# Performance work log

Hardware: AMD Instinct MI355X
Metric: run time of the kernel (lower is better)

## Reference

```python
import jax, jax.numpy as jnp
import numpy as np


def setup_inputs() -> dict:
    key = jax.random.key(0)
    ks = jax.random.split(key, 8)
    B, C, H, W = 32, 98, 128, 128
    F, D = 256, 128
    return {
        "hm": jax.random.normal(ks[0], (B, C, H, W), dtype=jnp.float32),
        "feat": jax.random.normal(ks[1], (B, F, H, W), dtype=jnp.float32),
        "W_embed": jax.random.normal(ks[2], (2 + 1 + F, D), dtype=jnp.float32) * 0.05,
        "b_embed": jax.random.normal(ks[3], (D,), dtype=jnp.float32) * 0.05,
        "A": jax.random.normal(ks[4], (C, C), dtype=jnp.float32) * 0.05,
        "W_gcn": jax.random.normal(ks[5], (D, D), dtype=jnp.float32) * 0.05,
        "W_out": jax.random.normal(ks[6], (D, 2), dtype=jnp.float32) * 0.05,
        "b_out": jax.random.normal(ks[7], (2,), dtype=jnp.float32) * 0.05,
    }


def reference(hm, feat, W_embed, b_embed, A, W_gcn, W_out, b_out):
    # hm: [B, C, H, W] per-landmark heatmaps; feat: [B, F, H, W] backbone features.
    B, C, H, W = hm.shape
    F = feat.shape[1]

    # decode_heatmap: per-(batch, landmark) argmax location over HxW (batched,
    # replacing the original per-sample Python loops).
    hm_flat = hm.reshape(B, C, H * W)
    idx = jnp.argmax(hm_flat, axis=-1)                      # [B, C] int
    ys = idx // W
    xs = idx % W

    # node confidences: hm[i, classIds, ys, xs] -> batched gather
    conf = jnp.take_along_axis(hm_flat, idx[:, :, None], axis=-1)[..., 0]  # [B, C]

    # pooling_feature: gather the F-dim feature vector at each landmark location
    feat_flat = feat.reshape(B, F, H * W)
    vis = jnp.take_along_axis(feat_flat, idx[:, None, :], axis=-1)  # [B, F, C]
    vis = jnp.transpose(vis, (0, 2, 1))                              # [B, C, F]

    # normalized positions: node_positions (x, y) / hm_size [h, w] (as in source)
    hm_size = jnp.array([H, W], dtype=hm.dtype)
    pos = jnp.stack([xs, ys], axis=-1).astype(hm.dtype) / hm_size    # [B, C, 2]

    # GCN over landmarks (batched instead of per-sample calls)
    node = jnp.concatenate([pos, conf[..., None], vis], axis=-1)     # [B, C, 2+1+F]
    h0 = jax.nn.relu(jnp.einsum("bcf,fd->bcd", node, W_embed) + b_embed)
    h1 = jax.nn.relu(jnp.einsum("ij,bjd,de->bie", A, h0, W_gcn))     # learned adjacency
    out = jnp.einsum("bcd,do->bco", h1, W_out) + b_out               # [B, C, 2]
    return hm, out
```

## Files before the change

### kernel.cpp

```cpp
#include <hip/hip_runtime.h>

#define HM_B 32
#define HM_C 98
#define HM_H 128
#define HM_W 128
#define HWSZ (HM_H * HM_W)
#define FDIM 256
#define DDIM 128
#define NODE_F (2 + 1 + FDIM)
#define BC (HM_B * HM_C)
#define HM_ELEMS ((size_t)BC * HWSZ)
#define LCHUNK 8
#define ICHUNK 7

typedef float f32x4 __attribute__((ext_vector_type(4)));

__global__ __launch_bounds__(256) void argmax_copy_kernel(
    const float* __restrict__ hm, float* __restrict__ out_hm,
    int* __restrict__ idx_ws, float* __restrict__ conf_ws) {
    const int bc = blockIdx.x;
    const int tid = threadIdx.x;
    const f32x4* __restrict__ src = (const f32x4*)(hm + (size_t)bc * HWSZ);
    f32x4* __restrict__ dst = (f32x4*)(out_hm + (size_t)bc * HWSZ);

    float bv = -INFINITY;
    int bi = 0;
    #pragma unroll
    for (int t = 0; t < HWSZ / 4 / 256; ++t) {
        const int p = t * 256 + tid;
        const f32x4 v = __builtin_nontemporal_load(src + p);
        __builtin_nontemporal_store(v, dst + p);
        const float m4 = fmaxf(fmaxf(v[0], v[1]), fmaxf(v[2], v[3]));
        if (m4 > bv) {
            const int base = p * 4;
            if (v[0] > bv) { bv = v[0]; bi = base; }
            if (v[1] > bv) { bv = v[1]; bi = base + 1; }
            if (v[2] > bv) { bv = v[2]; bi = base + 2; }
            if (v[3] > bv) { bv = v[3]; bi = base + 3; }
        }
    }

    __shared__ float sv[256];
    __shared__ int si[256];
    sv[tid] = bv; si[tid] = bi;
    __syncthreads();
    for (int s = 128; s > 0; s >>= 1) {
        if (tid < s) {
            const float ov = sv[tid + s];
            const int oi = si[tid + s];
            if (ov > sv[tid] || (ov == sv[tid] && oi < si[tid])) {
                sv[tid] = ov; si[tid] = oi;
            }
        }
        __syncthreads();
    }
    if (tid == 0) { idx_ws[bc] = si[0]; conf_ws[bc] = sv[0]; }
}

__global__ __launch_bounds__(256) void embed_kernel(
    const float* __restrict__ feat, const int* __restrict__ idx_ws,
    const float* __restrict__ conf_ws, const float* __restrict__ W_embed,
    const float* __restrict__ b_embed, float* __restrict__ h0) {
    const int bc0 = blockIdx.x * LCHUNK;
    const int tid = threadIdx.x;
    __shared__ float node_s[LCHUNK][NODE_F + 1];

    if (tid < LCHUNK) {
        const int bcL = bc0 + tid;
        const int loc = idx_ws[bcL];
        const int ys = loc / HM_W;
        const int xs = loc % HM_W;
        node_s[tid][0] = (float)xs / (float)HM_H;
        node_s[tid][1] = (float)ys / (float)HM_W;
        node_s[tid][2] = conf_ws[bcL];
    }
    #pragma unroll
    for (int l = 0; l < LCHUNK; ++l) {
        const int bcL = bc0 + l;
        const int b = bcL / HM_C;
        const int loc = idx_ws[bcL];
        node_s[l][3 + tid] = feat[((size_t)(b * FDIM + tid)) * HWSZ + loc];
    }
    __syncthreads();

    const int d = tid & (DDIM - 1);
    const int lbase = (tid >> 7) * 4;
    const float bias = b_embed[d];
    float acc0 = bias, acc1 = bias, acc2 = bias, acc3 = bias;
    for (int f = 0; f < NODE_F; ++f) {
        const float w = W_embed[f * DDIM + d];
        acc0 = fmaf(node_s[lbase + 0][f], w, acc0);
        acc1 = fmaf(node_s[lbase + 1][f], w, acc1);
        acc2 = fmaf(node_s[lbase + 2][f], w, acc2);
        acc3 = fmaf(node_s[lbase + 3][f], w, acc3);
    }
    h0[(size_t)(bc0 + lbase + 0) * DDIM + d] = fmaxf(acc0, 0.f);
    h0[(size_t)(bc0 + lbase + 1) * DDIM + d] = fmaxf(acc1, 0.f);
    h0[(size_t)(bc0 + lbase + 2) * DDIM + d] = fmaxf(acc2, 0.f);
    h0[(size_t)(bc0 + lbase + 3) * DDIM + d] = fmaxf(acc3, 0.f);
}

__global__ __launch_bounds__(128) void gcn_kernel(
    const float* __restrict__ A, const float* __restrict__ h0,
    const float* __restrict__ W_gcn, const float* __restrict__ W_out,
    const float* __restrict__ b_out, float* __restrict__ out2) {
    const int b = blockIdx.x / (HM_C / ICHUNK);
    const int i0 = (blockIdx.x % (HM_C / ICHUNK)) * ICHUNK;
    const int tid = threadIdx.x;

    __shared__ float h0_s[HM_C * DDIM];
    __shared__ float tmp_s[ICHUNK * DDIM];
    __shared__ float h1_s[ICHUNK * DDIM];

    for (int j = 0; j < HM_C; ++j)
        h0_s[j * DDIM + tid] = h0[((size_t)b * HM_C + j) * DDIM + tid];
    __syncthreads();

    {
        float acc[ICHUNK];
        #pragma unroll
        for (int i = 0; i < ICHUNK; ++i) acc[i] = 0.f;
        for (int j = 0; j < HM_C; ++j) {
            const float v = h0_s[j * DDIM + tid];
            #pragma unroll
            for (int i = 0; i < ICHUNK; ++i)
                acc[i] = fmaf(A[(i0 + i) * HM_C + j], v, acc[i]);
        }
        #pragma unroll
        for (int i = 0; i < ICHUNK; ++i) tmp_s[i * DDIM + tid] = acc[i];
    }
    __syncthreads();

    {
        float acc[ICHUNK];
        #pragma unroll
        for (int i = 0; i < ICHUNK; ++i) acc[i] = 0.f;
        for (int k = 0; k < DDIM; ++k) {
            const float w = W_gcn[k * DDIM + tid];
            #pragma unroll
            for (int i = 0; i < ICHUNK; ++i)
                acc[i] = fmaf(tmp_s[i * DDIM + k], w, acc[i]);
        }
        #pragma unroll
        for (int i = 0; i < ICHUNK; ++i) h1_s[i * DDIM + tid] = fmaxf(acc[i], 0.f);
    }
    __syncthreads();

    if (tid < ICHUNK * 2) {
        const int i = tid >> 1;
        const int o = tid & 1;
        float acc = b_out[o];
        for (int dd = 0; dd < DDIM; ++dd)
            acc = fmaf(h1_s[i * DDIM + dd], W_out[dd * 2 + o], acc);
        out2[((size_t)b * HM_C + i0 + i) * 2 + o] = acc;
    }
}

extern "C" void kernel_launch(void* const* d_in, const int* in_sizes, int n_in,
                              void* d_out, int out_size, void* d_ws, size_t ws_size,
                              hipStream_t stream) {
    const float* hm      = (const float*)d_in[0];
    const float* feat    = (const float*)d_in[1];
    const float* W_embed = (const float*)d_in[2];
    const float* b_embed = (const float*)d_in[3];
    const float* A       = (const float*)d_in[4];
    const float* W_gcn   = (const float*)d_in[5];
    const float* W_out   = (const float*)d_in[6];
    const float* b_out   = (const float*)d_in[7];

    float* out_hm = (float*)d_out;
    float* out2   = (float*)d_out + HM_ELEMS;

    char* ws = (char*)d_ws;
    int*   idx_ws  = (int*)ws;    ws += BC * sizeof(int);
    float* conf_ws = (float*)ws;  ws += BC * sizeof(float);
    float* h0      = (float*)ws;

    argmax_copy_kernel<<<BC, 256, 0, stream>>>(hm, out_hm, idx_ws, conf_ws);
    embed_kernel<<<BC / LCHUNK, 256, 0, stream>>>(feat, idx_ws, conf_ws,
                                                  W_embed, b_embed, h0);
    gcn_kernel<<<HM_B * (HM_C / ICHUNK), 128, 0, stream>>>(A, h0, W_gcn,
                                                           W_out, b_out, out2);
}
```

Measured before the change: 128.5 us.

## Fuse argmax, embed and GCN stages into one cooperative persistent kernel

Replaces three kernel launches with a single cooperative kernel of 512 persistent blocks that loops over heatmap rows, then uses grid-wide syncs between the argmax/copy, embedding and GCN phases. The aim is to remove launch gaps and tail effects between stages. The GCN stage no longer stages all of h0 in shared memory; it caches only the needed A rows and reads h0 from global memory, which cuts shared memory use. Nontemporal loads and stores in the copy are also replaced with plain ones. Risks include the cost of grid syncs, fewer blocks in flight for the large copy, and cache pollution from the normal stores. The original three launches remain as a fallback if the cooperative launch fails.

New measurement: 268.0 us. 2.09x slower.

```diff
diff --git a/kernel.cpp b/kernel.cpp
--- a/kernel.cpp
+++ b/kernel.cpp
@@ -1,4 +1,7 @@
 #include <hip/hip_runtime.h>
+#include <hip/hip_cooperative_groups.h>
+
+namespace cg = cooperative_groups;
 
 #define HM_B 32
 #define HM_C 98
@@ -12,24 +15,24 @@
 #define HM_ELEMS ((size_t)BC * HWSZ)
 #define LCHUNK 8
 #define ICHUNK 7
+#define NBLK 512
+#define NTHR 256
 
 typedef float f32x4 __attribute__((ext_vector_type(4)));
 
-__global__ __launch_bounds__(256) void argmax_copy_kernel(
-    const float* __restrict__ hm, float* __restrict__ out_hm,
-    int* __restrict__ idx_ws, float* __restrict__ conf_ws) {
-    const int bc = blockIdx.x;
-    const int tid = threadIdx.x;
-    const f32x4* __restrict__ src = (const f32x4*)(hm + (size_t)bc * HWSZ);
-    f32x4* __restrict__ dst = (f32x4*)(out_hm + (size_t)bc * HWSZ);
-
+
+__device__ __forceinline__ void argmax_copy_row(
+    const float* __restrict__ hm, float* __restrict__ out_hm, int row, int tid,
+    float* sv, int* si, int* __restrict__ idx_ws, float* __restrict__ conf_ws) {
+    const f32x4* __restrict__ src = (const f32x4*)(hm + (size_t)row * HWSZ);
+    f32x4* __restrict__ dst = (f32x4*)(out_hm + (size_t)row * HWSZ);
     float bv = -INFINITY;
     int bi = 0;
     #pragma unroll
-    for (int t = 0; t < HWSZ / 4 / 256; ++t) {
-        const int p = t * 256 + tid;
-        const f32x4 v = __builtin_nontemporal_load(src + p);
-        __builtin_nontemporal_store(v, dst + p);
+    for (int t = 0; t < HWSZ / 4 / NTHR; ++t) {
+        const int p = t * NTHR + tid;
+        const f32x4 v = src[p];
+        dst[p] = v;
         const float m4 = fmaxf(fmaxf(v[0], v[1]), fmaxf(v[2], v[3]));
         if (m4 > bv) {
             const int base = p * 4;
@@ -39,12 +42,9 @@
             if (v[3] > bv) { bv = v[3]; bi = base + 3; }
         }
     }
-
-    __shared__ float sv[256];
-    __shared__ int si[256];
     sv[tid] = bv; si[tid] = bi;
     __syncthreads();
-    for (int s = 128; s > 0; s >>= 1) {
+    for (int s = NTHR / 2; s > 0; s >>= 1) {
         if (tid < s) {
             const float ov = sv[tid + s];
             const int oi = si[tid + s];
@@ -54,32 +54,31 @@
         }
         __syncthreads();
     }
-    if (tid == 0) { idx_ws[bc] = si[0]; conf_ws[bc] = sv[0]; }
-}
-
-__global__ __launch_bounds__(256) void embed_kernel(
+    if (tid == 0) { idx_ws[row] = si[0]; conf_ws[row] = sv[0]; }
+    __syncthreads();
+}
+
+__device__ __forceinline__ void embed_unit(
     const float* __restrict__ feat, const int* __restrict__ idx_ws,
     const float* __restrict__ conf_ws, const float* __restrict__ W_embed,
-    const float* __restrict__ b_embed, float* __restrict__ h0) {
-    const int bc0 = blockIdx.x * LCHUNK;
-    const int tid = threadIdx.x;
-    __shared__ float node_s[LCHUNK][NODE_F + 1];
-
+    const float* __restrict__ b_embed, float* __restrict__ h0,
+    int unit, int tid, float (*node)[NODE_F + 1]) {
+    const int bc0 = unit * LCHUNK;
+    #pragma unroll
+    for (int l = 0; l < LCHUNK; ++l) {
+        const int bcL = bc0 + l;
+        const int b = bcL / HM_C;
+        const int loc = idx_ws[bcL];
+        node[l][3 + tid] = feat[((size_t)(b * FDIM + tid)) * HWSZ + loc];
+    }
     if (tid < LCHUNK) {
         const int bcL = bc0 + tid;
         const int loc = idx_ws[bcL];
         const int ys = loc / HM_W;
         const int xs = loc % HM_W;
-        node_s[tid][0] = (float)xs / (float)HM_H;
-        node_s[tid][1] = (float)ys / (float)HM_W;
-        node_s[tid][2] = conf_ws[bcL];
-    }
-    #pragma unroll
-    for (int l = 0; l < LCHUNK; ++l) {
-        const int bcL = bc0 + l;
-        const int b = bcL / HM_C;
-        const int loc = idx_ws[bcL];
-        node_s[l][3 + tid] = feat[((size_t)(b * FDIM + tid)) * HWSZ + loc];
+        node[tid][0] = (float)xs / (float)HM_H;
+        node[tid][1] = (float)ys / (float)HM_W;
+        node[tid][2] = conf_ws[bcL];
     }
     __syncthreads();
 
@@ -89,49 +88,49 @@
     float acc0 = bias, acc1 = bias, acc2 = bias, acc3 = bias;
     for (int f = 0; f < NODE_F; ++f) {
         const float w = W_embed[f * DDIM + d];
-        acc0 = fmaf(node_s[lbase + 0][f], w, acc0);
-        acc1 = fmaf(node_s[lbase + 1][f], w, acc1);
-        acc2 = fmaf(node_s[lbase + 2][f], w, acc2);
-        acc3 = fmaf(node_s[lbase + 3][f], w, acc3);
+        acc0 = fmaf(node[lbase + 0][f], w, acc0);
+        acc1 = fmaf(node[lbase + 1][f], w, acc1);
+        acc2 = fmaf(node[lbase + 2][f], w, acc2);
+        acc3 = fmaf(node[lbase + 3][f], w, acc3);
     }
     h0[(size_t)(bc0 + lbase + 0) * DDIM + d] = fmaxf(acc0, 0.f);
     h0[(size_t)(bc0 + lbase + 1) * DDIM + d] = fmaxf(acc1, 0.f);
     h0[(size_t)(bc0 + lbase + 2) * DDIM + d] = fmaxf(acc2, 0.f);
     h0[(size_t)(bc0 + lbase + 3) * DDIM + d] = fmaxf(acc3, 0.f);
-}
-
-__global__ __launch_bounds__(128) void gcn_kernel(
+    __syncthreads();
+}
+
+__device__ __forceinline__ void gcn_unit(
     const float* __restrict__ A, const float* __restrict__ h0,
     const float* __restrict__ W_gcn, const float* __restrict__ W_out,
-    const float* __restrict__ b_out, float* __restrict__ out2) {
-    const int b = blockIdx.x / (HM_C / ICHUNK);
-    const int i0 = (blockIdx.x % (HM_C / ICHUNK)) * ICHUNK;
-    const int tid = threadIdx.x;
-
-    __shared__ float h0_s[HM_C * DDIM];
-    __shared__ float tmp_s[ICHUNK * DDIM];
-    __shared__ float h1_s[ICHUNK * DDIM];
-
-    for (int j = 0; j < HM_C; ++j)
-        h0_s[j * DDIM + tid] = h0[((size_t)b * HM_C + j) * DDIM + tid];
-    __syncthreads();
-
-    {
+    const float* __restrict__ b_out, float* __restrict__ out2,
+    int unit, int tid, char* smraw) {
+    float* arow  = (float*)smraw;
+    float* tmp_s = (float*)(smraw + 2752);
+    float* h1_s  = (float*)(smraw + 2752 + 3584);
+    const int b = unit / (HM_C / ICHUNK);
+    const int i0 = (unit % (HM_C / ICHUNK)) * ICHUNK;
+
+    for (int k = tid; k < ICHUNK * HM_C; k += NTHR)
+        arow[k] = A[(i0 + k / HM_C) * HM_C + (k % HM_C)];
+    __syncthreads();
+
+    if (tid < DDIM) {
         float acc[ICHUNK];
         #pragma unroll
         for (int i = 0; i < ICHUNK; ++i) acc[i] = 0.f;
         for (int j = 0; j < HM_C; ++j) {
-            const float v = h0_s[j * DDIM + tid];
+            const float v = h0[((size_t)b * HM_C + j) * DDIM + tid];
             #pragma unroll
             for (int i = 0; i < ICHUNK; ++i)
-                acc[i] = fmaf(A[(i0 + i) * HM_C + j], v, acc[i]);
+                acc[i] = fmaf(arow[i * HM_C + j], v, acc[i]);
         }
         #pragma unroll
         for (int i = 0; i < ICHUNK; ++i) tmp_s[i * DDIM + tid] = acc[i];
     }
     __syncthreads();
 
-    {
+    if (tid < DDIM) {
         float acc[ICHUNK];
         #pragma unroll
         for (int i = 0; i < ICHUNK; ++i) acc[i] = 0.f;
@@ -154,6 +153,63 @@
             acc = fmaf(h1_s[i * DDIM + dd], W_out[dd * 2 + o], acc);
         out2[((size_t)b * HM_C + i0 + i) * 2 + o] = acc;
     }
+    __syncthreads();
+}
+
+
+__global__ __launch_bounds__(NTHR, 2) void fused_kernel(
+    const float* __restrict__ hm, const float* __restrict__ feat,
+    const float* __restrict__ W_embed, const float* __restrict__ b_embed,
+    const float* __restrict__ A, const float* __restrict__ W_gcn,
+    const float* __restrict__ W_out, const float* __restrict__ b_out,
+    float* __restrict__ out_hm, float* __restrict__ out2,
+    int* __restrict__ idx_ws, float* __restrict__ conf_ws,
+    float* __restrict__ h0_ws) {
+    cg::grid_group grid = cg::this_grid();
+    const int tid = threadIdx.x;
+    __shared__ __align__(16) char smraw[10240];
+
+    {
+        float* sv = (float*)smraw;
+        int* si = (int*)(smraw + NTHR * sizeof(float));
+        for (int row = blockIdx.x; row < BC; row += NBLK)
+            argmax_copy_row(hm, out_hm, row, tid, sv, si, idx_ws, conf_ws);
+    }
+    grid.sync();
+
+    if (blockIdx.x < BC / LCHUNK)
+        embed_unit(feat, idx_ws, conf_ws, W_embed, b_embed, h0_ws,
+                   blockIdx.x, tid, (float (*)[NODE_F + 1])smraw);
+    grid.sync();
+
+    if (blockIdx.x < HM_B * (HM_C / ICHUNK))
+        gcn_unit(A, h0_ws, W_gcn, W_out, b_out, out2, blockIdx.x, tid, smraw);
+}
+
+
+__global__ __launch_bounds__(NTHR) void argmax_copy_kernel(
+    const float* __restrict__ hm, float* __restrict__ out_hm,
+    int* __restrict__ idx_ws, float* __restrict__ conf_ws) {
+    __shared__ float sv[NTHR];
+    __shared__ int si[NTHR];
+    argmax_copy_row(hm, out_hm, blockIdx.x, threadIdx.x, sv, si, idx_ws, conf_ws);
+}
+
+__global__ __launch_bounds__(NTHR) void embed_kernel(
+    const float* __restrict__ feat, const int* __restrict__ idx_ws,
+    const float* __restrict__ conf_ws, const float* __restrict__ W_embed,
+    const float* __restrict__ b_embed, float* __restrict__ h0) {
+    __shared__ float node[LCHUNK][NODE_F + 1];
+    embed_unit(feat, idx_ws, conf_ws, W_embed, b_embed, h0,
+               blockIdx.x, threadIdx.x, node);
+}
+
+__global__ __launch_bounds__(NTHR) void gcn_kernel(
+    const float* __restrict__ A, const float* __restrict__ h0,
+    const float* __restrict__ W_gcn, const float* __restrict__ W_out,
+    const float* __restrict__ b_out, float* __restrict__ out2) {
+    __shared__ __align__(16) char smraw[10240];
+    gcn_unit(A, h0, W_gcn, W_out, b_out, out2, blockIdx.x, threadIdx.x, smraw);
 }
 
 extern "C" void kernel_launch(void* const* d_in, const int* in_sizes, int n_in,
@@ -174,11 +230,21 @@
     char* ws = (char*)d_ws;
     int*   idx_ws  = (int*)ws;    ws += BC * sizeof(int);
     float* conf_ws = (float*)ws;  ws += BC * sizeof(float);
-    float* h0      = (float*)ws;
-
-    argmax_copy_kernel<<<BC, 256, 0, stream>>>(hm, out_hm, idx_ws, conf_ws);
-    embed_kernel<<<BC / LCHUNK, 256, 0, stream>>>(feat, idx_ws, conf_ws,
-                                                  W_embed, b_embed, h0);
-    gcn_kernel<<<HM_B * (HM_C / ICHUNK), 128, 0, stream>>>(A, h0, W_gcn,
-                                                           W_out, b_out, out2);
-}
+    float* h0_ws   = (float*)ws;
+
+    void* args[] = {(void*)&hm, (void*)&feat, (void*)&W_embed, (void*)&b_embed,
+                    (void*)&A, (void*)&W_gcn, (void*)&W_out, (void*)&b_out,
+                    (void*)&out_hm, (void*)&out2, (void*)&idx_ws, (void*)&conf_ws,
+                    (void*)&h0_ws};
+    hipError_t err = hipLaunchCooperativeKernel(
+        reinterpret_cast<void*>(fused_kernel), dim3(NBLK), dim3(NTHR),
+        args, 0, stream);
+
+    if (err != hipSuccess) {
+        argmax_copy_kernel<<<BC, NTHR, 0, stream>>>(hm, out_hm, idx_ws, conf_ws);
+        embed_kernel<<<BC / LCHUNK, NTHR, 0, stream>>>(feat, idx_ws, conf_ws,
+                                                       W_embed, b_embed, h0_ws);
+        gcn_kernel<<<HM_B * (HM_C / ICHUNK), NTHR, 0, stream>>>(
+            A, h0_ws, W_gcn, W_out, b_out, out2);
+    }
+}
```

## Fuse feature gather into argmax kernel and stage A rows in GCN shared memory

Applied to the files above, without the earlier changes.

The argmax/copy kernel now gathers the 256-dim feature vector at the argmax location itself and writes a full padded node row (position, confidence, features) to a workspace. The embed kernel then only loads these rows, and writes h0 back into the first 128 slots of the same rows. The GCN kernel drops the 50 KB shared-memory copy of h0, which should raise occupancy. It caches the block's rows of A in shared memory and reads h0 directly from global memory instead. In exchange, each argmax block ends with a tail of scattered feature loads, and the GCN's h0 reads go to global or cache instead of LDS.

After: 127.7 us. Within noise of the previous version (-0.6%).

```diff
diff --git a/kernel.cpp b/kernel.cpp
--- a/kernel.cpp
+++ b/kernel.cpp
@@ -8,26 +8,28 @@
 #define FDIM 256
 #define DDIM 128
 #define NODE_F (2 + 1 + FDIM)
+#define NODE_P 260
 #define BC (HM_B * HM_C)
 #define HM_ELEMS ((size_t)BC * HWSZ)
 #define LCHUNK 8
 #define ICHUNK 7
+#define NTHR 256
 
 typedef float f32x4 __attribute__((ext_vector_type(4)));
 
-__global__ __launch_bounds__(256) void argmax_copy_kernel(
-    const float* __restrict__ hm, float* __restrict__ out_hm,
-    int* __restrict__ idx_ws, float* __restrict__ conf_ws) {
-    const int bc = blockIdx.x;
+__global__ __launch_bounds__(NTHR) void k1_copy_argmax_gather(
+    const float* __restrict__ hm, const float* __restrict__ feat,
+    float* __restrict__ out_hm, float* __restrict__ node_ws) {
+    const int row = blockIdx.x;
     const int tid = threadIdx.x;
-    const f32x4* __restrict__ src = (const f32x4*)(hm + (size_t)bc * HWSZ);
-    f32x4* __restrict__ dst = (f32x4*)(out_hm + (size_t)bc * HWSZ);
+    const f32x4* __restrict__ src = (const f32x4*)(hm + (size_t)row * HWSZ);
+    f32x4* __restrict__ dst = (f32x4*)(out_hm + (size_t)row * HWSZ);
 
     float bv = -INFINITY;
     int bi = 0;
     #pragma unroll
-    for (int t = 0; t < HWSZ / 4 / 256; ++t) {
-        const int p = t * 256 + tid;
+    for (int t = 0; t < HWSZ / 4 / NTHR; ++t) {
+        const int p = t * NTHR + tid;
         const f32x4 v = __builtin_nontemporal_load(src + p);
         __builtin_nontemporal_store(v, dst + p);
         const float m4 = fmaxf(fmaxf(v[0], v[1]), fmaxf(v[2], v[3]));
@@ -40,11 +42,11 @@
         }
     }
 
-    __shared__ float sv[256];
-    __shared__ int si[256];
+    __shared__ float sv[NTHR];
+    __shared__ int si[NTHR];
     sv[tid] = bv; si[tid] = bi;
     __syncthreads();
-    for (int s = 128; s > 0; s >>= 1) {
+    for (int s = NTHR / 2; s > 0; s >>= 1) {
         if (tid < s) {
             const float ov = sv[tid + s];
             const int oi = si[tid + s];
@@ -54,66 +56,64 @@
         }
         __syncthreads();
     }
-    if (tid == 0) { idx_ws[bc] = si[0]; conf_ws[bc] = sv[0]; }
+
+    const int loc = si[0];
+    const float conf = sv[0];
+    const int b = row / HM_C;
+    const float vis = feat[((size_t)(b * FDIM + tid)) * HWSZ + loc];
+    float* nrow = node_ws + (size_t)row * NODE_P;
+    nrow[3 + tid] = vis;
+    if (tid == 0) {
+        nrow[0] = (float)(loc % HM_W) * (1.0f / (float)HM_H);
+        nrow[1] = (float)(loc / HM_W) * (1.0f / (float)HM_W);
+        nrow[2] = conf;
+    }
 }
 
-__global__ __launch_bounds__(256) void embed_kernel(
-    const float* __restrict__ feat, const int* __restrict__ idx_ws,
-    const float* __restrict__ conf_ws, const float* __restrict__ W_embed,
-    const float* __restrict__ b_embed, float* __restrict__ h0) {
+__global__ __launch_bounds__(NTHR) void k2_embed(
+    float* __restrict__ node_ws, const float* __restrict__ W_embed,
+    const float* __restrict__ b_embed) {
     const int bc0 = blockIdx.x * LCHUNK;
     const int tid = threadIdx.x;
-    __shared__ float node_s[LCHUNK][NODE_F + 1];
+    __shared__ float node_s[LCHUNK][NODE_P];
 
-    if (tid < LCHUNK) {
-        const int bcL = bc0 + tid;
-        const int loc = idx_ws[bcL];
-        const int ys = loc / HM_W;
-        const int xs = loc % HM_W;
-        node_s[tid][0] = (float)xs / (float)HM_H;
-        node_s[tid][1] = (float)ys / (float)HM_W;
-        node_s[tid][2] = conf_ws[bcL];
-    }
     #pragma unroll
-    for (int l = 0; l < LCHUNK; ++l) {
-        const int bcL = bc0 + l;
-        const int b = bcL / HM_C;
-        const int loc = idx_ws[bcL];
-        node_s[l][3 + tid] = feat[((size_t)(b * FDIM + tid)) * HWSZ + loc];
-    }
+    for (int l = 0; l < LCHUNK; ++l)
+        for (int k = tid; k < NODE_F; k += NTHR)
+            node_s[l][k] = node_ws[(size_t)(bc0 + l) * NODE_P + k];
     __syncthreads();
 
     const int d = tid & (DDIM - 1);
     const int lbase = (tid >> 7) * 4;
     const float bias = b_embed[d];
-    float acc0 = bias, acc1 = bias, acc2 = bias, acc3 = bias;
+    float a0 = bias, a1 = bias, a2 = bias, a3 = bias;
     for (int f = 0; f < NODE_F; ++f) {
         const float w = W_embed[f * DDIM + d];
-        acc0 = fmaf(node_s[lbase + 0][f], w, acc0);
-        acc1 = fmaf(node_s[lbase + 1][f], w, acc1);
-        acc2 = fmaf(node_s[lbase + 2][f], w, acc2);
-        acc3 = fmaf(node_s[lbase + 3][f], w, acc3);
+        a0 = fmaf(node_s[lbase + 0][f], w, a0);
+        a1 = fmaf(node_s[lbase + 1][f], w, a1);
+        a2 = fmaf(node_s[lbase + 2][f], w, a2);
+        a3 = fmaf(node_s[lbase + 3][f], w, a3);
     }
-    h0[(size_t)(bc0 + lbase + 0) * DDIM + d] = fmaxf(acc0, 0.f);
-    h0[(size_t)(bc0 + lbase + 1) * DDIM + d] = fmaxf(acc1, 0.f);
-    h0[(size_t)(bc0 + lbase + 2) * DDIM + d] = fmaxf(acc2, 0.f);
-    h0[(size_t)(bc0 + lbase + 3) * DDIM + d] = fmaxf(acc3, 0.f);
+    node_ws[(size_t)(bc0 + lbase + 0) * NODE_P + d] = fmaxf(a0, 0.f);
+    node_ws[(size_t)(bc0 + lbase + 1) * NODE_P + d] = fmaxf(a1, 0.f);
+    node_ws[(size_t)(bc0 + lbase + 2) * NODE_P + d] = fmaxf(a2, 0.f);
+    node_ws[(size_t)(bc0 + lbase + 3) * NODE_P + d] = fmaxf(a3, 0.f);
 }
 
-__global__ __launch_bounds__(128) void gcn_kernel(
-    const float* __restrict__ A, const float* __restrict__ h0,
+__global__ __launch_bounds__(DDIM) void k3_gcn(
+    const float* __restrict__ A, const float* __restrict__ node_ws,
     const float* __restrict__ W_gcn, const float* __restrict__ W_out,
     const float* __restrict__ b_out, float* __restrict__ out2) {
     const int b = blockIdx.x / (HM_C / ICHUNK);
     const int i0 = (blockIdx.x % (HM_C / ICHUNK)) * ICHUNK;
     const int tid = threadIdx.x;
 
-    __shared__ float h0_s[HM_C * DDIM];
+    __shared__ float arow[ICHUNK * HM_C];
     __shared__ float tmp_s[ICHUNK * DDIM];
     __shared__ float h1_s[ICHUNK * DDIM];
 
-    for (int j = 0; j < HM_C; ++j)
-        h0_s[j * DDIM + tid] = h0[((size_t)b * HM_C + j) * DDIM + tid];
+    for (int k = tid; k < ICHUNK * HM_C; k += DDIM)
+        arow[k] = A[(i0 + k / HM_C) * HM_C + (k % HM_C)];
     __syncthreads();
 
     {
@@ -121,10 +121,10 @@
         #pragma unroll
         for (int i = 0; i < ICHUNK; ++i) acc[i] = 0.f;
         for (int j = 0; j < HM_C; ++j) {
-            const float v = h0_s[j * DDIM + tid];
+            const float v = node_ws[((size_t)b * HM_C + j) * NODE_P + tid];
             #pragma unroll
             for (int i = 0; i < ICHUNK; ++i)
-                acc[i] = fmaf(A[(i0 + i) * HM_C + j], v, acc[i]);
+                acc[i] = fmaf(arow[i * HM_C + j], v, acc[i]);
         }
         #pragma unroll
         for (int i = 0; i < ICHUNK; ++i) tmp_s[i * DDIM + tid] = acc[i];
@@ -171,14 +171,10 @@
     float* out_hm = (float*)d_out;
     float* out2   = (float*)d_out + HM_ELEMS;
 
-    char* ws = (char*)d_ws;
-    int*   idx_ws  = (int*)ws;    ws += BC * sizeof(int);
-    float* conf_ws = (float*)ws;  ws += BC * sizeof(float);
-    float* h0      = (float*)ws;
+    float* node_ws = (float*)d_ws;
 
-    argmax_copy_kernel<<<BC, 256, 0, stream>>>(hm, out_hm, idx_ws, conf_ws);
-    embed_kernel<<<BC / LCHUNK, 256, 0, stream>>>(feat, idx_ws, conf_ws,
-                                                  W_embed, b_embed, h0);
-    gcn_kernel<<<HM_B * (HM_C / ICHUNK), 128, 0, stream>>>(A, h0, W_gcn,
-                                                           W_out, b_out, out2);
+    k1_copy_argmax_gather<<<BC, NTHR, 0, stream>>>(hm, feat, out_hm, node_ws);
+    k2_embed<<<BC / LCHUNK, NTHR, 0, stream>>>(node_ws, W_embed, b_embed);
+    k3_gcn<<<HM_B * (HM_C / ICHUNK), DDIM, 0, stream>>>(A, node_ws, W_gcn,
+                                                        W_out, b_out, out2);
 }
```
